# Kernel optimization log

Measured on AMD Instinct MI355X. Metric: run time of the kernel, lower is better.

The kernel has to match this reference:

```python
import jax, jax.numpy as jnp
import numpy as np

B, T, C = 2, 2048, 1024
HS, DS = 8, 32      # short heads, short qk dim
HL, DL = 8, 128     # long heads, long qk dim
HD = 64             # value/output head dim = n_embd // n_head
WIN_S, WIN_L = 256, 1024
NEG = jnp.finfo(jnp.float32).min


def _window_mask(t, window):
    # additive mask: disallow future (i<j) and tokens older than the window
    i = jnp.arange(t)[:, None]
    j = jnp.arange(t)[None, :]
    bad = (i - j < 0) | (i - j >= window)
    return bad.astype(jnp.float32) * NEG  # [T,T]


def _attn(x, Wqk, Wv, n_h, d_qk, d_v, window):
    b, t, _ = x.shape
    qk = x @ Wqk                                      # [B,T,2*n_h*d_qk]
    q, k = jnp.split(qk, 2, axis=-1)
    q = q.reshape(b, t, n_h, d_qk).transpose(0, 2, 1, 3)  # [B,H,T,dqk]
    k = k.reshape(b, t, n_h, d_qk).transpose(0, 2, 1, 3)
    v = (x @ Wv).reshape(b, t, n_h, d_v).transpose(0, 2, 1, 3)  # [B,H,T,dv]
    scale = 1.0 / jnp.sqrt(jnp.float32(d_qk))
    scores = jnp.einsum('bhqd,bhkd->bhqk', q, k) * scale
    scores = scores + _window_mask(t, window)
    p = jax.nn.softmax(scores, axis=-1)
    return jnp.einsum('bhqk,bhkd->bhqd', p, v)        # [B,H,T,dv]


def setup_inputs() -> dict:
    key = jax.random.key(0)
    ks = jax.random.split(key, 6)
    s = 0.02
    return {
        'x': jax.random.normal(ks[0], (B, T, C), dtype=jnp.float32),
        'Wqk_short': jax.random.normal(ks[1], (C, 2 * HS * DS), dtype=jnp.float32) * s,
        'Wv_short': jax.random.normal(ks[2], (C, HS * HD), dtype=jnp.float32) * s,
        'Wqk_long': jax.random.normal(ks[3], (C, 2 * HL * DL), dtype=jnp.float32) * s,
        'Wv_long': jax.random.normal(ks[4], (C, HL * HD), dtype=jnp.float32) * s,
        'Wproj': jax.random.normal(ks[5], (C, C), dtype=jnp.float32) * s,
    }


def reference(x, Wqk_short, Wv_short, Wqk_long, Wv_long, Wproj):
    b, t, c = x.shape
    y_short = _attn(x, Wqk_short, Wv_short, HS, DS, HD, WIN_S)  # [B,HS,T,HD]
    y_long = _attn(x, Wqk_long, Wv_long, HL, DL, HD, WIN_L)     # [B,HL,T,HD]
    y = jnp.concatenate([y_short, y_long], axis=1)              # [B,H,T,HD]
    y = y.transpose(0, 2, 1, 3).reshape(b, t, c)
    return y @ Wproj
```

## Files before the change

kernel.cpp:

```cpp
#include <hip/hip_runtime.h>
#include <math.h>

#define B_    2
#define T_    2048
#define C_    1024
#define HS_   8
#define DS_   32
#define HL_   8
#define DL_   128
#define HD_   64
#define WINS_ 256
#define WINL_ 1024
#define NALL_ 3584

typedef __bf16 bf16x8 __attribute__((ext_vector_type(8)));
typedef float floatx4 __attribute__((ext_vector_type(4)));

__device__ __forceinline__ ushort f2bf(float f) {
    union { float f; unsigned u; } v; v.f = f;
    unsigned r = v.u + 0x7fff + ((v.u >> 16) & 1);
    return (ushort)(r >> 16);
}
__device__ __forceinline__ float bf2f(ushort u) {
    union { unsigned u; float f; } v; v.u = ((unsigned)u) << 16;
    return v.f;
}

#define DPP_STEP(x, ctrl, op)                                                \
    {                                                                        \
        float _t = __builtin_bit_cast(                                       \
            float, __builtin_amdgcn_update_dpp(                              \
                       0, __builtin_bit_cast(int, (x)), (ctrl), 0xf, 0xf,    \
                       true));                                               \
        (x) = op((x), _t);                                                   \
    }
__device__ __forceinline__ float dpp_max16(float x) {
    DPP_STEP(x, 0xB1, fmaxf);
    DPP_STEP(x, 0x4E, fmaxf);
    DPP_STEP(x, 0x141, fmaxf);
    DPP_STEP(x, 0x140, fmaxf);
    return x;
}
__device__ __forceinline__ float dpp_add16(float x) {
#define FADD_(a, b) ((a) + (b))
    DPP_STEP(x, 0xB1, FADD_);
    DPP_STEP(x, 0x4E, FADD_);
    DPP_STEP(x, 0x141, FADD_);
    DPP_STEP(x, 0x140, FADD_);
#undef FADD_
    return x;
}

__device__ __forceinline__ void gload_lds16(const void* g, void* l) {
    __builtin_amdgcn_global_load_lds(
        (const __attribute__((address_space(1))) void*)g,
        (__attribute__((address_space(3))) void*)l, 16, 0, 0);
}

__global__ __launch_bounds__(256) void prep(
    const float* __restrict__ x, ushort* __restrict__ x16,
    const float* __restrict__ Wqk_s, const float* __restrict__ Wv_s,
    const float* __restrict__ Wqk_l, const float* __restrict__ Wv_l,
    const float* __restrict__ Wproj, ushort* __restrict__ WallT,
    ushort* __restrict__ WprojT) {
    __shared__ float t[32][33];
    int bid = blockIdx.x;
    if (bid < 4096) {
        const int i = bid * 256 + threadIdx.x;
        float4 v = ((const float4*)x)[i];
        ushort4 o;
        o.x = f2bf(v.x); o.y = f2bf(v.y); o.z = f2bf(v.z); o.w = f2bf(v.w);
        ((ushort4*)x16)[i] = o;
        return;
    }
    bid -= 4096;
    const float* W; ushort* WT; int N, rowoff;
    if (bid < 512)       { W = Wqk_s; WT = WallT;  N = 512;  rowoff = 0; }
    else if (bid < 1024) { bid -= 512;  W = Wv_s;  WT = WallT;  N = 512;  rowoff = 512; }
    else if (bid < 3072) { bid -= 1024; W = Wqk_l; WT = WallT;  N = 2048; rowoff = 1024; }
    else if (bid < 3584) { bid -= 3072; W = Wv_l;  WT = WallT;  N = 512;  rowoff = 3072; }
    else                 { bid -= 3584; W = Wproj; WT = WprojT; N = 1024; rowoff = 0; }
    const int nt = N / 32;
    const int n0 = (bid % nt) * 32;
    const int k0 = (bid / nt) * 32;
    const int tx = threadIdx.x & 31;
    const int ty = threadIdx.x >> 5;
#pragma unroll
    for (int i = 0; i < 4; ++i)
        t[ty + 8 * i][tx] = W[(size_t)(k0 + ty + 8 * i) * N + n0 + tx];
    __syncthreads();
#pragma unroll
    for (int i = 0; i < 4; ++i)
        WT[(size_t)(rowoff + n0 + ty + 8 * i) * 1024 + k0 + tx] =
            f2bf(t[tx][ty + 8 * i]);
}

template <int BM, int BN, typename OT, bool FUSEV>
__global__ __launch_bounds__(256) void gemm_bf16(const ushort* __restrict__ A,
                                                 const ushort* __restrict__ BT,
                                                 OT* __restrict__ Cm,
                                                 ushort* __restrict__ VT,
                                                 int M, int N, int K) {
    __shared__ ushort As[3][BM * 32];
    __shared__ ushort Bs[3][BN * 32];
    constexpr int NI = BM / 32;
    constexpr int JB = BN / 32;
    const int tid = threadIdx.x;
    const int m0 = blockIdx.y * BM;
    const int n0 = blockIdx.x * BN;
    const int wave = tid >> 6;
    const int lane = tid & 63;
    const int wm = (wave >> 1) * (BM / 2);
    const int wn = (wave & 1) * (BN / 2);
    const int l15 = lane & 15;
    const int quad = lane >> 4;

    const int srow = tid >> 2;
    const int sc = (tid & 3) * 8;

    floatx4 acc[NI][JB] = {};

    const ushort* Ap0 = A + (size_t)(m0 + srow) * K + sc;
    const ushort* Ap1 = A + (size_t)(m0 + (srow & 63) + 64) * K + sc;
    const ushort* Bp0 = BT + (size_t)(n0 + srow) * K + sc;
    const ushort* Bp1 = BT + (size_t)(n0 + srow + 64) * K + sc;

    const int aoff0 = wave * 512;
    const int aoff1 = (wave * 512 + 2048) % (BM * 32);
    const int boff0 = wave * 512;
    const int boff1 = (wave * 512 + 2048) % (BN * 32);

#define STAGE(buf, kt)                                                     \
    {                                                                      \
        gload_lds16(Ap0 + (kt), &As[buf][aoff0]);                          \
        if constexpr (BM == 128) gload_lds16(Ap1 + (kt), &As[buf][aoff1]); \
        gload_lds16(Bp0 + (kt), &Bs[buf][boff0]);                          \
        if constexpr (BN == 128) gload_lds16(Bp1 + (kt), &Bs[buf][boff1]); \
    }

#define COMPUTE(buf)                                                       \
    {                                                                      \
        bf16x8 af[NI], bfr[JB];                                            \
        _Pragma("unroll") for (int i = 0; i < NI; ++i) af[i] =             \
            *(const bf16x8*)&As[buf][(wm + i * 16 + l15) * 32 + quad * 8]; \
        _Pragma("unroll") for (int j = 0; j < JB; ++j) bfr[j] =            \
            *(const bf16x8*)&Bs[buf][(wn + j * 16 + l15) * 32 + quad * 8]; \
        _Pragma("unroll") for (int i = 0; i < NI; ++i)                     \
            _Pragma("unroll") for (int j = 0; j < JB; ++j) acc[i][j] =     \
                __builtin_amdgcn_mfma_f32_16x16x32_bf16(af[i], bfr[j],     \
                                                        acc[i][j], 0, 0, 0); \
    }

#define WAIT_CUR()                                                    \
    {                                                                 \
        if constexpr (BM / 64 + BN / 64 == 4)                         \
            asm volatile("s_waitcnt vmcnt(4)" ::: "memory");          \
        else if constexpr (BM / 64 + BN / 64 == 3)                    \
            asm volatile("s_waitcnt vmcnt(3)" ::: "memory");          \
        else                                                          \
            asm volatile("s_waitcnt vmcnt(2)" ::: "memory");          \
    }

    STAGE(0, 0);
    STAGE(1, 32);
    int cur = 0;
    for (int kt = 0; kt + 32 < K; kt += 32) {
        WAIT_CUR();
        __builtin_amdgcn_s_barrier();
        __builtin_amdgcn_sched_barrier(0);
        if (kt + 64 < K) {
            int nxt2 = cur + 2;
            if (nxt2 >= 3) nxt2 -= 3;
            STAGE(nxt2, kt + 64);
        }
        COMPUTE(cur);
        ++cur;
        if (cur == 3) cur = 0;
    }
    asm volatile("s_waitcnt vmcnt(0)" ::: "memory");
    __builtin_amdgcn_s_barrier();
    __builtin_amdgcn_sched_barrier(0);
    COMPUTE(cur);
#undef STAGE
#undef COMPUTE
#undef WAIT_CUR

    bool vtile = false;
    if constexpr (FUSEV)
        vtile = (n0 >= 512 && n0 < 1024) || (n0 >= 3072);

    if (FUSEV && vtile) {
#pragma unroll
        for (int i = 0; i < NI; ++i) {
            const int m = m0 + wm + i * 16 + quad * 4;
            const int bb = m >> 11;
            const int t = m & 2047;
#pragma unroll
            for (int j = 0; j < JB; ++j) {
                const int col = n0 + wn + j * 16 + l15;
                const int vcol = (col < 1024) ? (col - 512) : (col - 2560);
                ushort4 val;
                val.x = f2bf(acc[i][j][0]);
                val.y = f2bf(acc[i][j][1]);
                val.z = f2bf(acc[i][j][2]);
                val.w = f2bf(acc[i][j][3]);
                *(ushort4*)&VT[((size_t)(bb * 1024 + vcol)) * T_ + t] = val;
            }
        }
    } else {
#pragma unroll
        for (int i = 0; i < NI; ++i)
#pragma unroll
            for (int j = 0; j < JB; ++j)
#pragma unroll
                for (int r = 0; r < 4; ++r) {
                    const size_t idx =
                        (size_t)(m0 + wm + i * 16 + quad * 4 + r) * N + n0 +
                        wn + j * 16 + l15;
                    if constexpr (sizeof(OT) == 2)
                        Cm[idx] = f2bf(acc[i][j][r]);
                    else
                        Cm[idx] = acc[i][j][r];
                }
    }
}

template <int D, int WIN, bool SPLIT>
__device__ __forceinline__ void attn_dev(
    const ushort* __restrict__ act, const ushort* __restrict__ vt,
    ushort* __restrict__ y, ushort* __restrict__ po, float* __restrict__ pm,
    float* __restrict__ pl, float scale2, int qoff, int koff, int head_off,
    int h, int gh, int b, int t0, int zs, ushort* lds) {
    constexpr int STR = D + 8;
    constexpr int PSTR = 72;
    constexpr int NKS = D / 32;
    constexpr int QCH = D / 8;
    constexpr int NKLD = (64 * QCH) / 256;

    ushort* Ks = lds;
    ushort* VTs = Ks + 64 * STR;
    ushort* Ps = VTs + 64 * PSTR;

    const int tid = threadIdx.x;
    const int wave = tid >> 6;
    const int lane = tid & 63;
    const int l15 = lane & 15;
    const int quad = lane >> 4;
    const int qmin = t0 + wave * 16;

    int k0s = t0 - WIN + 1;
    if (k0s < 0) k0s = 0;
    k0s &= ~63;

    int ks_begin = k0s, ks_last = t0;
    if (SPLIT) {
        const int nt = ((t0 - k0s) >> 6) + 1;
        const int ntlo = (nt + 1) >> 1;
        if (zs == 0) {
            ks_last = k0s + (ntlo - 1) * 64;
        } else {
            if (ntlo >= nt) {
#pragma unroll
                for (int r = 0; r < 4; ++r) {
                    const int t = qmin + quad * 4 + r;
                    const size_t ridx =
                        (((size_t)(zs * 2 + b) * 8 + h) * T_ + t);
                    if (l15 == 0) { pm[ridx] = -1e30f; pl[ridx] = 0.f; }
#pragma unroll
                    for (int j = 0; j < 4; ++j)
                        po[ridx * 64 + j * 16 + l15] = 0;
                }
                return;
            }
            ks_begin = k0s + ntlo * 64;
        }
    }

    const ushort* qbase = act + (size_t)(b * T_ + t0) * NALL_ + qoff + h * D;
    const ushort* kbase = act + (size_t)(b * T_) * NALL_ + koff + h * D;
    const ushort* vtb = vt + (size_t)((b * 16 + gh) * HD_) * T_;

    int krow[NKLD], kch[NKLD];
#pragma unroll
    for (int i = 0; i < NKLD; ++i) {
        const int idx = tid + 256 * i;
        krow[i] = idx / QCH;
        kch[i] = idx % QCH;
    }
    const int vd0 = tid >> 3, vc0 = (tid & 7) * 8;
    const int vd1 = (tid + 256) >> 3, vc1 = ((tid + 256) & 7) * 8;

    int4 kreg[NKLD], vreg0, vreg1;
#pragma unroll
    for (int i = 0; i < NKLD; ++i)
        kreg[i] = *(const int4*)(kbase + (size_t)(ks_begin + krow[i]) * NALL_ +
                                 kch[i] * 8);
    vreg0 = *(const int4*)(vtb + (size_t)vd0 * T_ + ks_begin + vc0);
    vreg1 = *(const int4*)(vtb + (size_t)vd1 * T_ + ks_begin + vc1);

    for (int idx = tid; idx < 64 * QCH; idx += 256) {
        const int row = idx / QCH;
        const int ch = idx % QCH;
        *(int4*)&Ks[row * STR + ch * 8] =
            *(const int4*)(qbase + (size_t)row * NALL_ + ch * 8);
    }
    __syncthreads();
    bf16x8 qa[NKS];
#pragma unroll
    for (int ks = 0; ks < NKS; ++ks)
        qa[ks] = *(const bf16x8*)&Ks[(wave * 16 + l15) * STR + ks * 32 + quad * 8];

    float m_i[4], l_i[4];
    floatx4 o_acc[4] = {};
#pragma unroll
    for (int r = 0; r < 4; ++r) { m_i[r] = -1e30f; l_i[r] = 0.f; }

    for (int k0 = ks_begin; k0 <= ks_last; k0 += 64) {
        __syncthreads();
#pragma unroll
        for (int i = 0; i < NKLD; ++i)
            *(int4*)&Ks[krow[i] * STR + kch[i] * 8] = kreg[i];
        *(int4*)&VTs[vd0 * PSTR + vc0] = vreg0;
        *(int4*)&VTs[vd1 * PSTR + vc1] = vreg1;
        __syncthreads();
        if (k0 + 64 <= ks_last) {
#pragma unroll
            for (int i = 0; i < NKLD; ++i)
                kreg[i] = *(const int4*)(kbase +
                                         (size_t)(k0 + 64 + krow[i]) * NALL_ +
                                         kch[i] * 8);
            vreg0 = *(const int4*)(vtb + (size_t)vd0 * T_ + k0 + 64 + vc0);
            vreg1 = *(const int4*)(vtb + (size_t)vd1 * T_ + k0 + 64 + vc1);
        }

        floatx4 s[4] = {};
#pragma unroll
        for (int ks = 0; ks < NKS; ++ks) {
#pragma unroll
            for (int j = 0; j < 4; ++j) {
                const bf16x8 bb =
                    *(const bf16x8*)&Ks[(j * 16 + l15) * STR + ks * 32 + quad * 8];
                s[j] = __builtin_amdgcn_mfma_f32_16x16x32_bf16(qa[ks], bb, s[j],
                                                               0, 0, 0);
            }
        }

        const bool full = (k0 + 63 <= qmin) && ((qmin + 15) - k0 <= WIN - 1);
        if (full) {
#pragma unroll
            for (int j = 0; j < 4; ++j)
#pragma unroll
                for (int r = 0; r < 4; ++r) s[j][r] *= scale2;
        } else {
#pragma unroll
            for (int j = 0; j < 4; ++j) {
                const int kj = k0 + j * 16 + l15;
#pragma unroll
                for (int r = 0; r < 4; ++r) {
                    const int rel = (qmin + quad * 4 + r) - kj;
                    s[j][r] = (rel < 0 || rel >= WIN) ? -1e30f : s[j][r] * scale2;
                }
            }
        }

        float rm[4];
#pragma unroll
        for (int r = 0; r < 4; ++r) {
            float t = fmaxf(fmaxf(s[0][r], s[1][r]), fmaxf(s[2][r], s[3][r]));
            rm[r] = dpp_max16(t);
        }
        const bool need = (rm[0] > m_i[0] + 8.f) || (rm[1] > m_i[1] + 8.f) ||
                          (rm[2] > m_i[2] + 8.f) || (rm[3] > m_i[3] + 8.f);
        if (__any(need)) {
#pragma unroll
            for (int r = 0; r < 4; ++r) {
                const float mn = fmaxf(m_i[r], rm[r]);
                const float a = exp2f(m_i[r] - mn);
                m_i[r] = mn;
                l_i[r] *= a;
#pragma unroll
                for (int j = 0; j < 4; ++j) o_acc[j][r] *= a;
            }
        }
#pragma unroll
        for (int r = 0; r < 4; ++r) {
            float sum = 0.f;
#pragma unroll
            for (int j = 0; j < 4; ++j) {
                const float e = exp2f(s[j][r] - m_i[r]);
                sum += e;
                Ps[(wave * 16 + quad * 4 + r) * PSTR + j * 16 + l15] = f2bf(e);
            }
            sum = dpp_add16(sum);
            l_i[r] += sum;
        }

#pragma unroll
        for (int kks = 0; kks < 2; ++kks) {
            const bf16x8 pa =
                *(const bf16x8*)&Ps[(wave * 16 + l15) * PSTR + kks * 32 + quad * 8];
#pragma unroll
            for (int j = 0; j < 4; ++j) {
                const bf16x8 vb =
                    *(const bf16x8*)&VTs[(j * 16 + l15) * PSTR + kks * 32 + quad * 8];
                o_acc[j] = __builtin_amdgcn_mfma_f32_16x16x32_bf16(pa, vb, o_acc[j],
                                                                   0, 0, 0);
            }
        }
    }

    if (SPLIT) {
#pragma unroll
        for (int r = 0; r < 4; ++r) {
            const int t = qmin + quad * 4 + r;
            const size_t ridx = (((size_t)(zs * 2 + b) * 8 + h) * T_ + t);
            if (l15 == 0) { pm[ridx] = m_i[r]; pl[ridx] = l_i[r]; }
#pragma unroll
            for (int j = 0; j < 4; ++j)
                po[ridx * 64 + j * 16 + l15] = f2bf(o_acc[j][r]);
        }
    } else {
#pragma unroll
        for (int r = 0; r < 4; ++r) {
            const float inv = 1.f / l_i[r];
            ushort* yrow = y + (size_t)(b * T_ + qmin + quad * 4 + r) * C_ +
                           head_off + h * HD_;
#pragma unroll
            for (int j = 0; j < 4; ++j)
                yrow[j * 16 + l15] = f2bf(o_acc[j][r] * inv);
        }
    }
}

__global__ __launch_bounds__(256, 4) void attn_sched(
    const ushort* __restrict__ act, const ushort* __restrict__ vt,
    ushort* __restrict__ y, ushort* __restrict__ po, float* __restrict__ pm,
    float* __restrict__ pl) {
    extern __shared__ ushort smem[];
    int x = blockIdx.x;
    if (x < 1024) {
        const int zs = x & 1;
        const int b = (x >> 1) & 1;
        const int h = (x >> 2) & 7;
        const int t0 = (31 - (x >> 5)) * 64;
        attn_dev<DL_, WINL_, true>(act, vt, y, po, pm, pl,
                                   0.12752021352994164f,
                                   1024, 2048, 512, h, 8 + h, b, t0, zs, smem);
    } else {
        x -= 1024;
        const int b = x & 1;
        const int h = (x >> 1) & 7;
        const int t0 = (31 - (x >> 4)) * 64;
        attn_dev<DS_, WINS_, false>(act, vt, y, po, pm, pl,
                                    0.2550404270598833f,
                                    0, 256, 0, h, h, b, t0, 0, smem);
    }
}

__global__ __launch_bounds__(256) void combine(const ushort* __restrict__ po,
                                               const float* __restrict__ pm,
                                               const float* __restrict__ pl,
                                               ushort* __restrict__ y) {
    const int gid = blockIdx.x * 256 + threadIdx.x;
    const int row = gid >> 4;
    const int cg = (gid & 15) * 4;
    const int b = row >> 14;
    const int h = (row >> 11) & 7;
    const int t = row & 2047;

    const float m0 = pm[row], m1 = pm[32768 + row];
    const float l0 = pl[row], l1 = pl[32768 + row];
    const float m = fmaxf(m0, m1);
    const float e0 = exp2f(m0 - m);
    const float e1 = exp2f(m1 - m);
    const float inv = 1.f / (l0 * e0 + l1 * e1);

    const ushort4 o0 = *(const ushort4*)&po[(size_t)row * 64 + cg];
    const ushort4 o1 = *(const ushort4*)&po[((size_t)32768 + row) * 64 + cg];

    ushort4 r;
    r.x = f2bf((bf2f(o0.x) * e0 + bf2f(o1.x) * e1) * inv);
    r.y = f2bf((bf2f(o0.y) * e0 + bf2f(o1.y) * e1) * inv);
    r.z = f2bf((bf2f(o0.z) * e0 + bf2f(o1.z) * e1) * inv);
    r.w = f2bf((bf2f(o0.w) * e0 + bf2f(o1.w) * e1) * inv);
    *(ushort4*)&y[(size_t)(b * T_ + t) * C_ + 512 + h * 64 + cg] = r;
}

extern "C" void kernel_launch(void* const* d_in, const int* in_sizes, int n_in,
                              void* d_out, int out_size, void* d_ws,
                              size_t ws_size, hipStream_t stream) {
    const float* x         = (const float*)d_in[0];
    const float* Wqk_short = (const float*)d_in[1];
    const float* Wv_short  = (const float*)d_in[2];
    const float* Wqk_long  = (const float*)d_in[3];
    const float* Wv_long   = (const float*)d_in[4];
    const float* Wproj     = (const float*)d_in[5];
    float* out = (float*)d_out;

    const int M = B_ * T_;

    ushort* x16    = (ushort*)d_ws;
    ushort* WallT  = x16 + (size_t)M * C_;
    ushort* WprojT = WallT + (size_t)NALL_ * C_;
    ushort* yb16   = WprojT + (size_t)C_ * C_;
    ushort* act    = yb16 + (size_t)M * C_;
    ushort* vt     = act + (size_t)M * NALL_;
    ushort* po     = vt + (size_t)32 * HD_ * T_;
    float*  pm     = (float*)(po + (size_t)2 * 32768 * 64);
    float*  pl     = pm + (size_t)2 * 32768;

    dim3 blk(256);
    prep<<<dim3(8704), blk, 0, stream>>>(x, x16, Wqk_short, Wv_short, Wqk_long,
                                         Wv_long, Wproj, WallT, WprojT);

    gemm_bf16<128, 128, ushort, true>
        <<<dim3(NALL_ / 128, M / 128), blk, 0, stream>>>(x16, WallT, act, vt,
                                                         M, NALL_, C_);

    const int attn_lds = (64 * (DL_ + 8) + 64 * 72 * 2) * 2;
    attn_sched<<<dim3(1536), blk, attn_lds, stream>>>(act, vt, yb16, po, pm, pl);

    combine<<<dim3(2048), blk, 0, stream>>>(po, pm, pl, yb16);

    gemm_bf16<64, 64, float, false>
        <<<dim3(C_ / 64, M / 64), blk, 0, stream>>>(yb16, WprojT, out, nullptr,
                                                    M, C_, C_);
}
```

Measured before the change: 212.9 us.

## Enlarge QKV GEMM tile to 256x128 with 512 threads and unified LDS staging

Makes the bf16 GEMM generic over thread count, with a single shared LDS buffer holding both A and B tiles and a generic per-thread load loop. The QKV projection GEMM now uses 256x128 tiles with 8 waves, which raises data reuse per block and halves the number of blocks along M. It also adds a launch-bounds occupancy hint. The cost is fewer blocks (28x16=448) for the CUs and higher LDS and register use per block.

```diff
diff --git a/kernel.cpp b/kernel.cpp
--- a/kernel.cpp
+++ b/kernel.cpp
@@ -95,67 +95,66 @@
             f2bf(t[tx][ty + 8 * i]);
 }
 
-template <int BM, int BN, typename OT, bool FUSEV>
-__global__ __launch_bounds__(256) void gemm_bf16(const ushort* __restrict__ A,
-                                                 const ushort* __restrict__ BT,
-                                                 OT* __restrict__ Cm,
-                                                 ushort* __restrict__ VT,
-                                                 int M, int N, int K) {
-    __shared__ ushort As[3][BM * 32];
-    __shared__ ushort Bs[3][BN * 32];
-    constexpr int NI = BM / 32;
+template <int BM, int BN, int TH, typename OT, bool FUSEV>
+__global__ __launch_bounds__(TH, 4) void gemm_bf16(const ushort* __restrict__ A,
+                                                   const ushort* __restrict__ BT,
+                                                   OT* __restrict__ Cm,
+                                                   ushort* __restrict__ VT,
+                                                   int M, int N, int K) {
+    __shared__ ushort S[3][(BM + BN) * 32];
+    constexpr int WM = TH / 128;
+    constexpr int NI = BM / WM / 16;
     constexpr int JB = BN / 32;
+    constexpr int NLD = (BM + BN) * 4 / TH;
+
     const int tid = threadIdx.x;
     const int m0 = blockIdx.y * BM;
     const int n0 = blockIdx.x * BN;
     const int wave = tid >> 6;
     const int lane = tid & 63;
-    const int wm = (wave >> 1) * (BM / 2);
+    const int wm = (wave >> 1) * (BM / WM);
     const int wn = (wave & 1) * (BN / 2);
     const int l15 = lane & 15;
     const int quad = lane >> 4;
 
-    const int srow = tid >> 2;
-    const int sc = (tid & 3) * 8;
-
     floatx4 acc[NI][JB] = {};
 
-    const ushort* Ap0 = A + (size_t)(m0 + srow) * K + sc;
-    const ushort* Ap1 = A + (size_t)(m0 + (srow & 63) + 64) * K + sc;
-    const ushort* Bp0 = BT + (size_t)(n0 + srow) * K + sc;
-    const ushort* Bp1 = BT + (size_t)(n0 + srow + 64) * K + sc;
-
-    const int aoff0 = wave * 512;
-    const int aoff1 = (wave * 512 + 2048) % (BM * 32);
-    const int boff0 = wave * 512;
-    const int boff1 = (wave * 512 + 2048) % (BN * 32);
-
-#define STAGE(buf, kt)                                                     \
-    {                                                                      \
-        gload_lds16(Ap0 + (kt), &As[buf][aoff0]);                          \
-        if constexpr (BM == 128) gload_lds16(Ap1 + (kt), &As[buf][aoff1]); \
-        gload_lds16(Bp0 + (kt), &Bs[buf][boff0]);                          \
-        if constexpr (BN == 128) gload_lds16(Bp1 + (kt), &Bs[buf][boff1]); \
-    }
-
-#define COMPUTE(buf)                                                       \
-    {                                                                      \
-        bf16x8 af[NI], bfr[JB];                                            \
-        _Pragma("unroll") for (int i = 0; i < NI; ++i) af[i] =             \
-            *(const bf16x8*)&As[buf][(wm + i * 16 + l15) * 32 + quad * 8]; \
-        _Pragma("unroll") for (int j = 0; j < JB; ++j) bfr[j] =            \
-            *(const bf16x8*)&Bs[buf][(wn + j * 16 + l15) * 32 + quad * 8]; \
-        _Pragma("unroll") for (int i = 0; i < NI; ++i)                     \
-            _Pragma("unroll") for (int j = 0; j < JB; ++j) acc[i][j] =     \
-                __builtin_amdgcn_mfma_f32_16x16x32_bf16(af[i], bfr[j],     \
+    const ushort* sbase[NLD];
+#pragma unroll
+    for (int i = 0; i < NLD; ++i) {
+        const int idx = tid + TH * i;
+        const int row = idx >> 2;
+        const int ch = (idx & 3) * 8;
+        sbase[i] = (row < BM) ? A + (size_t)(m0 + row) * K + ch
+                              : BT + (size_t)(n0 + row - BM) * K + ch;
+    }
+
+#define STAGE(buf, kt)                                                      \
+    {                                                                       \
+        _Pragma("unroll") for (int i_ = 0; i_ < NLD; ++i_)                  \
+            gload_lds16(sbase[i_] + (kt),                                   \
+                        &S[buf][(wave * 64 + TH * i_) * 8]);                \
+    }
+
+#define COMPUTE(buf)                                                        \
+    {                                                                       \
+        bf16x8 af[NI], bfr[JB];                                             \
+        _Pragma("unroll") for (int i = 0; i < NI; ++i) af[i] =              \
+            *(const bf16x8*)&S[buf][(wm + i * 16 + l15) * 32 + quad * 8];   \
+        _Pragma("unroll") for (int j = 0; j < JB; ++j) bfr[j] =             \
+            *(const bf16x8*)&S[buf][(BM + wn + j * 16 + l15) * 32 +         \
+                                    quad * 8];                              \
+        _Pragma("unroll") for (int i = 0; i < NI; ++i)                      \
+            _Pragma("unroll") for (int j = 0; j < JB; ++j) acc[i][j] =      \
+                __builtin_amdgcn_mfma_f32_16x16x32_bf16(af[i], bfr[j],      \
                                                         acc[i][j], 0, 0, 0); \
     }
 
 #define WAIT_CUR()                                                    \
     {                                                                 \
-        if constexpr (BM / 64 + BN / 64 == 4)                         \
+        if constexpr (NLD == 4)                                       \
             asm volatile("s_waitcnt vmcnt(4)" ::: "memory");          \
-        else if constexpr (BM / 64 + BN / 64 == 3)                    \
+        else if constexpr (NLD == 3)                                  \
             asm volatile("s_waitcnt vmcnt(3)" ::: "memory");          \
         else                                                          \
             asm volatile("s_waitcnt vmcnt(2)" ::: "memory");          \
@@ -513,16 +512,16 @@
     prep<<<dim3(8704), blk, 0, stream>>>(x, x16, Wqk_short, Wv_short, Wqk_long,
                                          Wv_long, Wproj, WallT, WprojT);
 
-    gemm_bf16<128, 128, ushort, true>
-        <<<dim3(NALL_ / 128, M / 128), blk, 0, stream>>>(x16, WallT, act, vt,
-                                                         M, NALL_, C_);
+    gemm_bf16<256, 128, 512, ushort, true>
+        <<<dim3(NALL_ / 128, M / 256), dim3(512), 0, stream>>>(
+            x16, WallT, act, vt, M, NALL_, C_);
 
     const int attn_lds = (64 * (DL_ + 8) + 64 * 72 * 2) * 2;
     attn_sched<<<dim3(1536), blk, attn_lds, stream>>>(act, vt, yb16, po, pm, pl);
 
     combine<<<dim3(2048), blk, 0, stream>>>(po, pm, pl, yb16);
 
-    gemm_bf16<64, 64, float, false>
+    gemm_bf16<64, 64, 256, float, false>
         <<<dim3(C_ / 64, M / 64), blk, 0, stream>>>(yb16, WprojT, out, nullptr,
                                                     M, C_, C_);
 }
```

Result: faster. 201.3 us (-5.5%).
